# Optimization experiments

Hardware: AMD Instinct MI355X
Metric: run time of the kernel (lower is better)

The kernel has to match this reference:

```python
import jax, jax.numpy as jnp
import numpy as np

B, N, DIM = 8, 8192, 256
K, CDIM = 4096, 1024
COMMIT = 0.25


def setup_inputs() -> dict:
    key = jax.random.key(0)
    ks = jax.random.split(key, 4)
    x = jax.random.normal(ks[0], (B, N, DIM), dtype=jnp.float32)
    ln_g = jnp.ones((DIM,), jnp.float32)
    ln_b = jnp.zeros((DIM,), jnp.float32)
    w_pre = jax.random.normal(ks[1], (DIM, CDIM), jnp.float32) / np.sqrt(DIM)
    b_pre = jnp.zeros((CDIM,), jnp.float32)
    embed = jax.random.normal(ks[2], (K, CDIM), jnp.float32)
    w_post = jax.random.normal(ks[3], (CDIM, DIM), jnp.float32) / np.sqrt(CDIM)
    b_post = jnp.zeros((DIM,), jnp.float32)
    return {"x": x, "ln_g": ln_g, "ln_b": ln_b, "w_pre": w_pre, "b_pre": b_pre,
            "embed": embed, "w_post": w_post, "b_post": b_post}


def reference(x, ln_g, ln_b, w_pre, b_pre, embed, w_post, b_post):
    # LayerNorm over last dim (eps=1e-5, torch default)
    mu = jnp.mean(x, axis=-1, keepdims=True)
    var = jnp.mean((x - mu) ** 2, axis=-1, keepdims=True)
    xn = (x - mu) * jax.lax.rsqrt(var + 1e-5) * ln_g + ln_b
    # GELU (exact, erf-based as in torch default) then Linear dim->codebook_dim
    z_e = jax.nn.gelu(xn, approximate=False) @ w_pre + b_pre  # (B,N,CDIM)
    flat = z_e.reshape(-1, CDIM)                              # (B*N, CDIM)
    # squared euclidean distances to codebook, argmin, gather
    z_sq = jnp.sum(flat * flat, axis=1, keepdims=True)        # (BN,1)
    e_sq = jnp.sum(embed * embed, axis=1)                     # (K,)
    dist = z_sq - 2.0 * (flat @ embed.T) + e_sq[None, :]      # (BN,K)
    indices = jnp.argmin(dist, axis=1)                        # (BN,)
    z_q = embed[indices]                                      # (BN,CDIM)
    # commitment loss (z_q detached)
    commit = COMMIT * jnp.mean((flat - jax.lax.stop_gradient(z_q)) ** 2)
    # straight-through estimator
    z_q_st = flat + jax.lax.stop_gradient(z_q - flat)
    z_q_st = z_q_st.reshape(B, N, CDIM)
    quantized = z_q_st @ w_post + b_post                      # (B,N,DIM)
    return quantized, indices.reshape(B, N), commit
```

## Files before the change

kernel.cpp:

```cpp
#include <hip/hip_runtime.h>

#define BN_ROWS 65536
#define DIMX 256
#define CDIM 1024
#define KCODES 4096
#define NSP 16
#define CMARG 2.5f
#define RMARG 1.2f
#define FLT_BIG 3.402823466e+38f

static const size_t OFF_ESQ   = 0;
static const size_t OFF_IDXF  = 16384;
static const size_t OFF_CROW  = 278528;
static const size_t OFF_EPOST = 540672;
static const size_t OFF_EH    = 4734976;
static const size_t OFF_NFLAG = 13123584;
static const size_t OFF_FLAG  = 13123648;
static const size_t OFF_CAND  = 13385792;

typedef __attribute__((ext_vector_type(8))) short bf16x8;
typedef __attribute__((ext_vector_type(4))) float f32x4;

#define GLOAD_LDS16(gsrc, ldst)                                                \
  __builtin_amdgcn_global_load_lds(                                            \
      (const __attribute__((address_space(1))) void*)(gsrc),                   \
      (__attribute__((address_space(3))) void*)(ldst), 16, 0, 0)

__device__ inline unsigned short bf_rtn(float f) {
  unsigned u = __float_as_uint(f);
  unsigned r = (u + 0x7FFFu + ((u >> 16) & 1u)) >> 16;
  return (unsigned short)r;
}
__device__ inline unsigned fkey(float s) {
  unsigned b = __float_as_uint(s);
  return b ^ ((unsigned)((int)b >> 31) | 0x80000000u);
}
__device__ inline float keyinv(unsigned k) {
  unsigned b = (k & 0x80000000u) ? (k ^ 0x80000000u) : ~k;
  return __uint_as_float(b);
}

__global__ __launch_bounds__(256) void k_esq(const float* __restrict__ embed,
                                             float* __restrict__ e_sq) {
  const int t = threadIdx.x, wv = t >> 6, lane = t & 63;
  const int row = blockIdx.x * 4 + wv;
  const float* e = embed + (size_t)row * CDIM;
  float s = 0.f;
  for (int k = lane * 4; k < CDIM; k += 256) {
    float4 v = *(const float4*)(e + k);
    s = fmaf(v.x, v.x, s); s = fmaf(v.y, v.y, s);
    s = fmaf(v.z, v.z, s); s = fmaf(v.w, v.w, s);
  }
#pragma unroll
  for (int o = 32; o > 0; o >>= 1) s += __shfl_xor(s, o);
  if (lane == 0) e_sq[row] = s;
}

__global__ __launch_bounds__(256) void k_ehi(const float* __restrict__ embed,
                                             short* __restrict__ Eh) {
  const int t = threadIdx.x;
  const size_t row = blockIdx.x;
  float4 v = *(const float4*)(embed + row * CDIM + t * 4);
  *(short4*)(Eh + row * CDIM + t * 4) =
      make_short4((short)bf_rtn(v.x), (short)bf_rtn(v.y), (short)bf_rtn(v.z),
                  (short)bf_rtn(v.w));
}

__global__ __launch_bounds__(256) void k_ln_gelu_gemm(
    const float* __restrict__ x, const float* __restrict__ ln_g,
    const float* __restrict__ ln_b, const float* __restrict__ w_pre,
    const float* __restrict__ b_pre, float* __restrict__ zf,
    short* __restrict__ zh, int row0) {
  __shared__ float g[16][DIMX];
  const int t = threadIdx.x;
  const int lrow0 = blockIdx.x * 16;
  const int grow0 = row0 + lrow0;
  const int wv = t >> 6, lane = t & 63;
#pragma unroll
  for (int j = 0; j < 4; ++j) {
    const int r = wv * 4 + j;
    const float* xr = x + (size_t)(grow0 + r) * DIMX;
    float4 v = *(const float4*)(xr + lane * 4);
    float s = v.x + v.y + v.z + v.w;
    float ss = v.x * v.x + v.y * v.y + v.z * v.z + v.w * v.w;
#pragma unroll
    for (int o = 32; o > 0; o >>= 1) { s += __shfl_xor(s, o); ss += __shfl_xor(ss, o); }
    const float mu = s * (1.0f / 256.0f);
    const float var = ss * (1.0f / 256.0f) - mu * mu;
    const float rstd = rsqrtf(var + 1e-5f);
    float vv[4] = {v.x, v.y, v.z, v.w};
#pragma unroll
    for (int q = 0; q < 4; ++q) {
      const int d = lane * 4 + q;
      float xn = (vv[q] - mu) * rstd * ln_g[d] + ln_b[d];
      g[r][d] = 0.5f * xn * (1.0f + erff(xn * 0.70710678118654752f));
    }
  }
  __syncthreads();
  float acc[16][4];
#pragma unroll
  for (int r = 0; r < 16; ++r)
#pragma unroll
    for (int c = 0; c < 4; ++c) acc[r][c] = 0.f;
#pragma unroll 4
  for (int d = 0; d < DIMX; ++d) {
    float4 w = *(const float4*)(w_pre + (size_t)d * CDIM + t * 4);
#pragma unroll
    for (int r = 0; r < 16; ++r) {
      const float gv = g[r][d];
      acc[r][0] = fmaf(gv, w.x, acc[r][0]);
      acc[r][1] = fmaf(gv, w.y, acc[r][1]);
      acc[r][2] = fmaf(gv, w.z, acc[r][2]);
      acc[r][3] = fmaf(gv, w.w, acc[r][3]);
    }
  }
  float4 bp = *(const float4*)(b_pre + t * 4);
#pragma unroll
  for (int r = 0; r < 16; ++r) {
    float4 o;
    o.x = acc[r][0] + bp.x; o.y = acc[r][1] + bp.y;
    o.z = acc[r][2] + bp.z; o.w = acc[r][3] + bp.w;
    *(float4*)(zf + (size_t)(lrow0 + r) * CDIM + t * 4) = o;
    *(short4*)(zh + (size_t)(lrow0 + r) * CDIM + t * 4) =
        make_short4((short)bf_rtn(o.x), (short)bf_rtn(o.y), (short)bf_rtn(o.z),
                    (short)bf_rtn(o.w));
  }
}

__global__ __launch_bounds__(512) void k_score(
    const short* __restrict__ Eh, const short* __restrict__ Zh,
    const float* __restrict__ e_sq, uint2* __restrict__ cand, int chunk) {
  __shared__ __align__(16) short lds[2][16384];
  const int t = threadIdx.x;
  const int cpx = gridDim.x >> 3;
  const int bx = (blockIdx.x & 7) * cpx + (blockIdx.x >> 3);
  const int zblk = bx / NSP, csp = bx % NSP;
  const int wid = t >> 6, l = t & 63;
  const int wr = wid >> 2, wc = wid & 3;
  const int lg = l >> 4, lo16 = l & 15;
  const int rowbase = zblk * 256;
  const int m0 = csp * 256;
  const int wr8 = wr * 8, wc4 = wc * 4, l8 = l * 8;

  const bool isA = (wid < 4);
  const int q = wid & 3;
  const short* sarr = isA ? Eh : Zh;
  const int sbase = isA ? m0 : rowbase;
  const short* sp0 = sarr + (size_t)(sbase + q * 64 + lo16) * 1024 + lg * 8;
  const int dstbase = (isA ? 0 : 8192) + q * 4 * 512;

  f32x4 acc[8][4];
#pragma unroll
  for (int mi = 0; mi < 8; ++mi)
#pragma unroll
    for (int ni = 0; ni < 4; ++ni) acc[mi][ni] = (f32x4){0.f, 0.f, 0.f, 0.f};

#pragma unroll
  for (int u = 0; u < 4; ++u)
    GLOAD_LDS16(sp0 + u * 16384, &lds[0][dstbase + u * 512]);
  asm volatile("s_waitcnt vmcnt(0)" ::: "memory");
  __builtin_amdgcn_s_barrier();
  __builtin_amdgcn_sched_barrier(0);

  for (int kt = 0; kt < 32; ++kt) {
    const int cur = kt & 1;
    const short* Lc = lds[cur];
    short* Dst = &lds[cur ^ 1][dstbase];
    const short* spk = sp0 + (kt + 1) * 32;
    const bool st = (kt < 31);

    bf16x8 bh[4];
#pragma unroll
    for (int ni = 0; ni < 4; ++ni)
      bh[ni] = *(const bf16x8*)(Lc + 8192 + (wc4 + ni) * 512 + l8);

#pragma unroll
    for (int p = 0; p < 2; ++p) {
      const int mi0 = 4 * p;
      bf16x8 a[4];
#pragma unroll
      for (int u = 0; u < 4; ++u)
        a[u] = *(const bf16x8*)(Lc + (wr8 + mi0 + u) * 512 + l8);
      if (p == 0 && st) {
#pragma unroll
        for (int u = 0; u < 4; ++u)
          GLOAD_LDS16(spk + u * 16384, Dst + u * 512);
      }
      __builtin_amdgcn_s_barrier();
      asm volatile("s_waitcnt lgkmcnt(0)" ::: "memory");
      __builtin_amdgcn_sched_barrier(0);
      __builtin_amdgcn_s_setprio(1);
#pragma unroll
      for (int u = 0; u < 4; ++u)
#pragma unroll
        for (int ni = 0; ni < 4; ++ni)
          acc[mi0 + u][ni] = __builtin_amdgcn_mfma_f32_16x16x32_bf16(
              a[u], bh[ni], acc[mi0 + u][ni], 0, 0, 0);
      __builtin_amdgcn_s_setprio(0);
      if (p == 1) asm volatile("s_waitcnt vmcnt(0)" ::: "memory");
      __builtin_amdgcn_s_barrier();
      __builtin_amdgcn_sched_barrier(0);
    }
  }

  float s1[4];
  int i1[4];
#pragma unroll
  for (int i = 0; i < 4; ++i) { s1[i] = FLT_BIG; i1[i] = 0x7fffffff; }
#pragma unroll
  for (int mi = 0; mi < 8; ++mi) {
    const int c0 = m0 + wr * 128 + mi * 16 + lg * 4;
    float4 es = *(const float4*)(e_sq + c0);
    float esv[4] = {es.x, es.y, es.z, es.w};
#pragma unroll
    for (int ni = 0; ni < 4; ++ni) {
#pragma unroll
      for (int j = 0; j < 4; ++j) {
        const float s = fmaf(-2.0f, acc[mi][ni][j], esv[j]);
        const int c = c0 + j;
        if (s < s1[ni] || (s == s1[ni] && c < i1[ni])) { s1[ni] = s; i1[ni] = c; }
      }
    }
  }

  unsigned long long* red = (unsigned long long*)&lds[0][0];
  float* sb = (float*)&lds[0][2048];
  unsigned* sbi = (unsigned*)&lds[0][2560];
  unsigned* cnt = (unsigned*)&lds[0][3072];
  uint2* slot = (uint2*)&lds[0][3584];

#pragma unroll
  for (int ni = 0; ni < 4; ++ni) {
    unsigned long long k1v =
        (((unsigned long long)fkey(s1[ni])) << 32) | (unsigned)i1[ni];
    unsigned long long o1 = __shfl_xor(k1v, 16);
    k1v = o1 < k1v ? o1 : k1v;
    o1 = __shfl_xor(k1v, 32);
    k1v = o1 < k1v ? o1 : k1v;
    if (lg == 0) {
      const int r = wc * 64 + ni * 16 + lo16;
      red[r * 2 + wr] = k1v;
    }
  }
  __syncthreads();
  if (t < 256) {
    unsigned long long a1 = red[t * 2 + 0], b1 = red[t * 2 + 1];
    if (b1 < a1) a1 = b1;
    sb[t] = keyinv((unsigned)(a1 >> 32));
    sbi[t] = (unsigned)(a1 & 0xFFFFFFFFull);
    cnt[t] = 0;
  }
  __syncthreads();
#pragma unroll
  for (int mi = 0; mi < 8; ++mi) {
    const int c0 = m0 + wr * 128 + mi * 16 + lg * 4;
    float4 es = *(const float4*)(e_sq + c0);
    float esv[4] = {es.x, es.y, es.z, es.w};
#pragma unroll
    for (int ni = 0; ni < 4; ++ni) {
      const int r = wc * 64 + ni * 16 + lo16;
      const float thr = sb[r] + CMARG;
#pragma unroll
      for (int j = 0; j < 4; ++j) {
        const float s = fmaf(-2.0f, acc[mi][ni][j], esv[j]);
        const unsigned c = (unsigned)(c0 + j);
        if (s < thr && c != sbi[r]) {
          unsigned pos = atomicAdd(&cnt[r], 1u);
          if (pos < 3) slot[r * 3 + pos] = make_uint2(__float_as_uint(s), c);
        }
      }
    }
  }
  __syncthreads();
  if (t < 256) {
    uint2* g = cand + ((size_t)(rowbase + t) * NSP + csp) * 4;
    const unsigned ov = (cnt[t] > 3) ? 0x40000000u : 0u;
    g[0] = make_uint2(__float_as_uint(sb[t]), sbi[t] | ov);
    const unsigned n = cnt[t] > 3 ? 3 : cnt[t];
#pragma unroll
    for (int k = 0; k < 3; ++k)
      g[1 + k] = (k < (int)n) ? slot[t * 3 + k]
                              : make_uint2(__float_as_uint(FLT_BIG), 0xFFFFFFFFu);
  }
}

__global__ __launch_bounds__(256) void k_refine(
    const uint2* __restrict__ cand, const float* __restrict__ zf,
    const float* __restrict__ embed, int* __restrict__ idxf,
    float* __restrict__ crow, float* __restrict__ out_idx,
    int* __restrict__ flag_rows, int* __restrict__ nflag, int chunk,
    int row0) {
  const int t = threadIdx.x, wid = t >> 6, l = t & 63;
  const int lrow = blockIdx.x * 4 + wid;
  if (lrow >= chunk) return;
  const int grow = row0 + lrow;
  const uint2 cs = cand[(size_t)lrow * 64 + l];
  const float sc = __uint_as_float(cs.x);
  const unsigned raw = cs.y;
  const bool isMin = (l & 3) == 0;
  float gm = isMin ? sc : FLT_BIG;
#pragma unroll
  for (int o = 32; o > 0; o >>= 1) gm = fminf(gm, __shfl_xor(gm, o));
  const float thr = gm + RMARG;
  const bool ovf = __any(isMin && (raw & 0x40000000u) && (sc < thr));

  float zv[16];
#pragma unroll
  for (int j = 0; j < 16; ++j) zv[j] = zf[(size_t)lrow * CDIM + l + 64 * j];

  const int myidx = (int)(raw & 0xFFFFu);
  const bool valid = (sc < thr) && (myidx < KCODES);
  unsigned long long mask = __ballot(valid);
  double d1 = 1e300;
  int i1 = 0x7fffffff;
  while (mask) {
    const int src = __ffsll((unsigned long long)mask) - 1;
    mask &= mask - 1;
    const int c = __shfl(myidx, src);
    const float* e = embed + (size_t)c * CDIM;
    double dd = 0.0;
#pragma unroll
    for (int j = 0; j < 16; ++j) {
      const double df = (double)zv[j] - (double)e[l + 64 * j];
      dd = fma(df, df, dd);
    }
#pragma unroll
    for (int o = 32; o > 0; o >>= 1) dd += __shfl_xor(dd, o);
    if (dd < d1 || (dd == d1 && c < i1)) { d1 = dd; i1 = c; }
  }
  if (l == 0) {
    idxf[grow] = i1;
    out_idx[grow] = (float)i1;
    crow[grow] = (float)d1;
    if (ovf) {
      const int s = atomicAdd(nflag, 1);
      flag_rows[s] = lrow;
    }
  }
}

__global__ __launch_bounds__(256) void k_exact(
    const float* __restrict__ zf, const float* __restrict__ embed,
    const int* __restrict__ flag_rows, const int* __restrict__ nflag,
    int* __restrict__ idxf, float* __restrict__ crow,
    float* __restrict__ out_idx, int row0) {
  __shared__ double wd[4];
  __shared__ int wcidx[4];
  const int t = threadIdx.x;
  const int wid = t >> 6, l = t & 63;
  const int n = *nflag;

  for (int fi = blockIdx.x; fi < n; fi += gridDim.x) {
    const int lrow = flag_rows[fi];
    const int grow = row0 + lrow;
    float zr[16];
#pragma unroll
    for (int j = 0; j < 16; ++j) zr[j] = zf[(size_t)lrow * CDIM + l + 64 * j];
    double dmin = 1e300;
    int cmin = 0x7fffffff;
    for (int ci = 0; ci < 1024; ++ci) {
      const int c = wid * 1024 + ci;
      const float* e = embed + (size_t)c * CDIM;
      double dd = 0.0;
#pragma unroll
      for (int j = 0; j < 16; ++j) {
        const double df = (double)zr[j] - (double)e[l + 64 * j];
        dd = fma(df, df, dd);
      }
#pragma unroll
      for (int o = 32; o > 0; o >>= 1) dd += __shfl_xor(dd, o);
      if (dd < dmin) { dmin = dd; cmin = c; }
    }
    if (l == 0) { wd[wid] = dmin; wcidx[wid] = cmin; }
    __syncthreads();
    if (t == 0) {
      double dm = wd[0]; int cm = wcidx[0];
#pragma unroll
      for (int wv = 1; wv < 4; ++wv) {
        if (wd[wv] < dm || (wd[wv] == dm && wcidx[wv] < cm)) {
          dm = wd[wv]; cm = wcidx[wv];
        }
      }
      idxf[grow] = cm;
      out_idx[grow] = (float)cm;
      crow[grow] = (float)dm;
    }
    __syncthreads();
  }
}

__global__ __launch_bounds__(256) void k_epost(const float* __restrict__ E,
                                               const float* __restrict__ w_post,
                                               float* __restrict__ E_post) {
  __shared__ float es[16][128];
  const int t = threadIdx.x;
  const int r0 = blockIdx.x * 16;
  float acc[16];
#pragma unroll
  for (int r = 0; r < 16; ++r) acc[r] = 0.f;
  for (int k0 = 0; k0 < CDIM; k0 += 128) {
    __syncthreads();
#pragma unroll
    for (int p = 0; p < 2; ++p) {
      const int fl = (p * 256 + t) * 4;
      const int r = fl >> 7, kk = fl & 127;
      float4 v = *(const float4*)(E + (size_t)(r0 + r) * CDIM + k0 + kk);
      *(float4*)&es[r][kk] = v;
    }
    __syncthreads();
#pragma unroll 4
    for (int d = 0; d < 128; ++d) {
      const float w = w_post[(size_t)(k0 + d) * DIMX + t];
#pragma unroll
      for (int r = 0; r < 16; ++r) acc[r] = fmaf(es[r][d], w, acc[r]);
    }
  }
#pragma unroll
  for (int r = 0; r < 16; ++r)
    E_post[(size_t)(r0 + r) * DIMX + t] = acc[r];
}

__global__ __launch_bounds__(256) void k_gather(const float* __restrict__ E_post,
                                                const int* __restrict__ idx,
                                                const float* __restrict__ b_post,
                                                float* __restrict__ outq) {
  const int t = threadIdx.x;
  const int r0 = blockIdx.x * 16;
  const float bp = b_post[t];
#pragma unroll
  for (int i = 0; i < 16; ++i) {
    const int row = r0 + i;
    outq[(size_t)row * DIMX + t] = E_post[(size_t)idx[row] * DIMX + t] + bp;
  }
}

__global__ __launch_bounds__(256) void k_commit_final(
    const float* __restrict__ crow, float* __restrict__ out_commit) {
  const int t = threadIdx.x;
  double s = 0.0;
  for (int i = t; i < BN_ROWS; i += 256) s += (double)crow[i];
#pragma unroll
  for (int o = 32; o > 0; o >>= 1) s += __shfl_xor(s, o);
  __shared__ double wsum[4];
  if ((t & 63) == 0) wsum[t >> 6] = s;
  __syncthreads();
  if (t == 0)
    *out_commit = (float)(0.25 * (wsum[0] + wsum[1] + wsum[2] + wsum[3]) /
                          (65536.0 * 1024.0));
}

extern "C" void kernel_launch(void* const* d_in, const int* in_sizes, int n_in,
                              void* d_out, int out_size, void* d_ws,
                              size_t ws_size, hipStream_t stream) {
  const float* x = (const float*)d_in[0];
  const float* ln_g = (const float*)d_in[1];
  const float* ln_b = (const float*)d_in[2];
  const float* w_pre = (const float*)d_in[3];
  const float* b_pre = (const float*)d_in[4];
  const float* embed = (const float*)d_in[5];
  const float* w_post = (const float*)d_in[6];
  const float* b_post = (const float*)d_in[7];

  float* out = (float*)d_out;
  float* outq = out;
  float* out_idx = out + 16777216;
  float* out_commit = out + 16842752;

  char* ws = (char*)d_ws;
  float* e_sq = (float*)(ws + OFF_ESQ);
  int* idxf = (int*)(ws + OFF_IDXF);
  float* crow = (float*)(ws + OFF_CROW);
  float* E_post = (float*)(ws + OFF_EPOST);
  short* Eh = (short*)(ws + OFF_EH);
  int* nflag = (int*)(ws + OFF_NFLAG);
  int* flag_rows = (int*)(ws + OFF_FLAG);

  int chunk = 4096;
  while (chunk < BN_ROWS &&
         OFF_CAND + (size_t)(chunk * 2) * 6656ull <= ws_size)
    chunk *= 2;
  uint2* cand = (uint2*)(ws + OFF_CAND);
  short* zh = (short*)(ws + OFF_CAND + (size_t)chunk * 512);
  float* zf = (float*)(ws + OFF_CAND + (size_t)chunk * 512 + (size_t)chunk * 2048);

  k_esq<<<KCODES / 4, 256, 0, stream>>>(embed, e_sq);
  k_ehi<<<KCODES, 256, 0, stream>>>(embed, Eh);
  k_epost<<<KCODES / 16, 256, 0, stream>>>(embed, w_post, E_post);

  for (int row0 = 0; row0 < BN_ROWS; row0 += chunk) {
    hipMemsetAsync(nflag, 0, sizeof(int), stream);
    k_ln_gelu_gemm<<<chunk / 16, 256, 0, stream>>>(x, ln_g, ln_b, w_pre, b_pre,
                                                   zf, zh, row0);
    k_score<<<(chunk / 256) * NSP, 512, 0, stream>>>(Eh, zh, e_sq, cand, chunk);
    k_refine<<<chunk / 4, 256, 0, stream>>>(cand, zf, embed, idxf, crow,
                                            out_idx, flag_rows, nflag, chunk,
                                            row0);
    k_exact<<<128, 256, 0, stream>>>(zf, embed, flag_rows, nflag, idxf, crow,
                                     out_idx, row0);
  }

  k_gather<<<BN_ROWS / 16, 256, 0, stream>>>(E_post, idxf, b_post, outq);
  k_commit_final<<<1, 256, 0, stream>>>(crow, out_commit);
}
```

Before: 1.585 ms.

## Use a four-stage LDS ring with depth-3 prefetch in the score GEMM

Replaces the double-buffered K loop in the distance/score kernel with a four-buffer LDS ring. Loads run three k-steps ahead, and graded vmcnt waits retire only the oldest stage. Each k-step now uses one barrier instead of two, and all eight A fragments load at once before the MFMAs. The aim is to hide global-to-LDS latency and cut synchronisation stalls. The cost is double the LDS footprint (128KB per block), which likely allows only one 512-thread block per CU, plus more register pressure from the eight A fragments held at once.

```diff
diff --git a/kernel.cpp b/kernel.cpp
--- a/kernel.cpp
+++ b/kernel.cpp
@@ -25,6 +25,16 @@
   __builtin_amdgcn_global_load_lds(                                            \
       (const __attribute__((address_space(1))) void*)(gsrc),                   \
       (__attribute__((address_space(3))) void*)(ldst), 16, 0, 0)
+
+template <int VMC>
+__device__ __forceinline__ void wait_vm() {
+  if constexpr (VMC == 8)
+    asm volatile("s_waitcnt vmcnt(8)" ::: "memory");
+  else if constexpr (VMC == 4)
+    asm volatile("s_waitcnt vmcnt(4)" ::: "memory");
+  else
+    asm volatile("s_waitcnt vmcnt(0)" ::: "memory");
+}
 
 __device__ inline unsigned short bf_rtn(float f) {
   unsigned u = __float_as_uint(f);
@@ -130,7 +140,7 @@
 __global__ __launch_bounds__(512) void k_score(
     const short* __restrict__ Eh, const short* __restrict__ Zh,
     const float* __restrict__ e_sq, uint2* __restrict__ cand, int chunk) {
-  __shared__ __align__(16) short lds[2][16384];
+  __shared__ __align__(16) short lds[4][16384];
   const int t = threadIdx.x;
   const int cpx = gridDim.x >> 3;
   const int bx = (blockIdx.x & 7) * cpx + (blockIdx.x >> 3);
@@ -156,52 +166,44 @@
     for (int ni = 0; ni < 4; ++ni) acc[mi][ni] = (f32x4){0.f, 0.f, 0.f, 0.f};
 
 #pragma unroll
-  for (int u = 0; u < 4; ++u)
-    GLOAD_LDS16(sp0 + u * 16384, &lds[0][dstbase + u * 512]);
-  asm volatile("s_waitcnt vmcnt(0)" ::: "memory");
-  __builtin_amdgcn_s_barrier();
-  __builtin_amdgcn_sched_barrier(0);
-
-  for (int kt = 0; kt < 32; ++kt) {
-    const int cur = kt & 1;
-    const short* Lc = lds[cur];
-    short* Dst = &lds[cur ^ 1][dstbase];
-    const short* spk = sp0 + (kt + 1) * 32;
-    const bool st = (kt < 31);
-
-    bf16x8 bh[4];
-#pragma unroll
-    for (int ni = 0; ni < 4; ++ni)
-      bh[ni] = *(const bf16x8*)(Lc + 8192 + (wc4 + ni) * 512 + l8);
-
-#pragma unroll
-    for (int p = 0; p < 2; ++p) {
-      const int mi0 = 4 * p;
-      bf16x8 a[4];
-#pragma unroll
-      for (int u = 0; u < 4; ++u)
-        a[u] = *(const bf16x8*)(Lc + (wr8 + mi0 + u) * 512 + l8);
-      if (p == 0 && st) {
-#pragma unroll
-        for (int u = 0; u < 4; ++u)
-          GLOAD_LDS16(spk + u * 16384, Dst + u * 512);
-      }
-      __builtin_amdgcn_s_barrier();
-      asm volatile("s_waitcnt lgkmcnt(0)" ::: "memory");
-      __builtin_amdgcn_sched_barrier(0);
-      __builtin_amdgcn_s_setprio(1);
-#pragma unroll
-      for (int u = 0; u < 4; ++u)
-#pragma unroll
-        for (int ni = 0; ni < 4; ++ni)
-          acc[mi0 + u][ni] = __builtin_amdgcn_mfma_f32_16x16x32_bf16(
-              a[u], bh[ni], acc[mi0 + u][ni], 0, 0, 0);
-      __builtin_amdgcn_s_setprio(0);
-      if (p == 1) asm volatile("s_waitcnt vmcnt(0)" ::: "memory");
-      __builtin_amdgcn_s_barrier();
-      __builtin_amdgcn_sched_barrier(0);
-    }
-  }
+  for (int pk = 0; pk < 3; ++pk) {
+    const short* sp = sp0 + pk * 32;
+    short* D = &lds[pk][dstbase];
+#pragma unroll
+    for (int u = 0; u < 4; ++u) GLOAD_LDS16(sp + u * 16384, D + u * 512);
+  }
+
+#define SCORE_KT(KT, VMC, ST)                                                  \
+  {                                                                            \
+    const short* Lc = lds[(KT) & 3];                                           \
+    wait_vm<VMC>();                                                            \
+    __builtin_amdgcn_s_barrier();                                              \
+    __builtin_amdgcn_sched_barrier(0);                                         \
+    bf16x8 bh[4], a[8];                                                        \
+    _Pragma("unroll") for (int ni = 0; ni < 4; ++ni) bh[ni] =                  \
+        *(const bf16x8*)(Lc + 8192 + (wc4 + ni) * 512 + l8);                   \
+    _Pragma("unroll") for (int u = 0; u < 8; ++u) a[u] =                       \
+        *(const bf16x8*)(Lc + (wr8 + u) * 512 + l8);                           \
+    if (ST) {                                                                  \
+      short* Dst = &lds[((KT) + 3) & 3][dstbase];                              \
+      const short* spk = sp0 + ((KT) + 3) * 32;                                \
+      _Pragma("unroll") for (int u = 0; u < 4; ++u)                            \
+          GLOAD_LDS16(spk + u * 16384, Dst + u * 512);                         \
+    }                                                                          \
+    asm volatile("s_waitcnt lgkmcnt(0)" ::: "memory");                         \
+    __builtin_amdgcn_sched_barrier(0);                                         \
+    __builtin_amdgcn_s_setprio(1);                                             \
+    _Pragma("unroll") for (int u = 0; u < 8; ++u)                              \
+        _Pragma("unroll") for (int ni = 0; ni < 4; ++ni) acc[u][ni] =          \
+            __builtin_amdgcn_mfma_f32_16x16x32_bf16(a[u], bh[ni],              \
+                                                    acc[u][ni], 0, 0, 0);      \
+    __builtin_amdgcn_s_setprio(0);                                             \
+  }
+
+  for (int kt = 0; kt < 30; ++kt) SCORE_KT(kt, 8, (kt < 29));
+  SCORE_KT(30, 4, false);
+  SCORE_KT(31, 0, false);
+#undef SCORE_KT
 
   float s1[4];
   int i1[4];
@@ -229,6 +231,7 @@
   unsigned* cnt = (unsigned*)&lds[0][3072];
   uint2* slot = (uint2*)&lds[0][3584];
 
+  __syncthreads();
 #pragma unroll
   for (int ni = 0; ni < 4; ++ni) {
     unsigned long long k1v =
```

Measured after the change: 1.456 ms. 8.2% less time.
